# Kernel tuning notes

Measured on AMD Instinct MI355X. Metric: run time of the kernel, lower is better.

Reference implementation:

```python
import jax, jax.numpy as jnp
import numpy as np

B, T, E, D = 8, 2048, 1024, 128  # batch, seq, embedding_dim, head_dim


def setup_inputs() -> dict:
    key = jax.random.key(0)
    ks = jax.random.split(key, 7)
    s = 1.0 / np.sqrt(E)  # torch Linear default init scale
    return {
        "x": jax.random.normal(ks[0], (B, T, E), dtype=jnp.float32),
        "Wq": jax.random.uniform(ks[1], (E, D), jnp.float32, -s, s),
        "bq": jax.random.uniform(ks[2], (D,), jnp.float32, -s, s),
        "Wk": jax.random.uniform(ks[3], (E, D), jnp.float32, -s, s),
        "bk": jax.random.uniform(ks[4], (D,), jnp.float32, -s, s),
        "Wv": jax.random.uniform(ks[5], (E, D), jnp.float32, -s, s),
        "bv": jax.random.uniform(ks[6], (D,), jnp.float32, -s, s),
        "mask": 1,
    }


def reference(x, Wq, bq, Wk, bk, Wv, bv, mask):
    # Q/K/V projections: [B,T,E] @ [E,D] -> [B,T,D]
    q = x @ Wq + bq
    k = x @ Wk + bk
    v = x @ Wv + bv
    d_k = q.shape[-1]
    # scores: [B,T,T]
    scores = jnp.einsum("btd,bsd->bts", q, k) / jnp.sqrt(jnp.float32(d_k))
    if mask:  # causal masked_fill with -inf (static python flag)
        causal = jnp.tril(jnp.ones((q.shape[1], q.shape[1]), dtype=bool))
        scores = jnp.where(causal[None, :, :], scores, -jnp.inf)
    att = jax.nn.softmax(scores, axis=-1)
    # dropout p=0.0 (inference) -> identity
    return jnp.einsum("bts,bsd->btd", att, v)
```

## Files before the change

### kernel.cpp

```cpp
#include <hip/hip_runtime.h>
#include <hip/hip_bf16.h>

#define BSZ  8
#define TSEQ 2048
#define EDIM 1024
#define DDIM 128
#define MROWS (BSZ * TSEQ)
#define NQT  (TSEQ / 64)

typedef __attribute__((ext_vector_type(8))) __bf16 bf16x8;
typedef __attribute__((ext_vector_type(4))) __bf16 bf16x4;
typedef __attribute__((ext_vector_type(2))) __bf16 bf16x2;
typedef __attribute__((ext_vector_type(4))) float f32x4;

__global__ __launch_bounds__(256) void wt_kernel(
    const float* __restrict__ Wq, const float* __restrict__ Wk,
    const float* __restrict__ Wv, __bf16* __restrict__ wt)
{
    const float* W = (blockIdx.y == 0) ? Wq : (blockIdx.y == 1) ? Wk : Wv;
    __bf16* o = wt + (size_t)blockIdx.y * DDIM * EDIM;
    const int k0 = blockIdx.x * 64;
    __shared__ __align__(16) __bf16 t[64][140];
    const int tid = threadIdx.x;
    #pragma unroll
    for (int i = 0; i < 8; ++i) {
        int idx = tid + i * 256;
        int k = idx >> 5, c4 = idx & 31;
        float4 v = *(const float4*)&W[(size_t)(k0 + k) * DDIM + c4 * 4];
        bf16x4 b4;
        b4[0] = (__bf16)v.x; b4[1] = (__bf16)v.y; b4[2] = (__bf16)v.z; b4[3] = (__bf16)v.w;
        *(bf16x4*)&t[k][c4 * 4] = b4;
    }
    __syncthreads();
    #pragma unroll
    for (int i = 0; i < 4; ++i) {
        int idx = tid + i * 256;
        int n = idx >> 3, c8 = idx & 7;
        bf16x8 r;
        #pragma unroll
        for (int u = 0; u < 8; ++u) r[u] = t[c8 * 8 + u][n];
        *(bf16x8*)&o[(size_t)n * EDIM + k0 + c8 * 8] = r;
    }
}

__global__ __launch_bounds__(256) void qkv_fused_kernel(
    const float* __restrict__ x, const __bf16* __restrict__ wt,
    const float* __restrict__ bq, const float* __restrict__ bk,
    const float* __restrict__ bv,
    __bf16* __restrict__ qo, __bf16* __restrict__ ko, __bf16* __restrict__ vto)
{
    const int bid = blockIdx.x;
    const int xcd = bid & 7;
    const int h   = (bid >> 3) & 3;
    const int mt  = (bid >> 5) * 8 + xcd;
    const int m0  = mt * 64;

    __shared__ __align__(16) __bf16 a_lds[64][72];
    __shared__ __align__(16) __bf16 b_lds[96][72];

    const int tid  = threadIdx.x;
    const int lane = tid & 63;
    const int wv   = tid >> 6;
    const int wr   = wv >> 1, wc = wv & 1;
    const int cl   = lane & 15, gr = lane >> 4;

    f32x4 acc[2][3] = {};

    float4 ra[4];
    bf16x8 rb[3];
    const int arow = tid >> 4,  ac4 = tid & 15;
    const int brow = tid >> 3,  bc8 = tid & 7;

#define LOADAB(K0) do {                                                        \
    _Pragma("unroll")                                                          \
    for (int i = 0; i < 4; ++i)                                                \
        ra[i] = *(const float4*)&x[(size_t)(m0 + arow + i * 16) * EDIM + (K0) + ac4 * 4]; \
    _Pragma("unroll")                                                          \
    for (int i = 0; i < 3; ++i)                                                \
        rb[i] = *(const bf16x8*)&wt[(size_t)(h * 96 + brow + i * 32) * EDIM + (K0) + bc8 * 8]; \
  } while (0)

    LOADAB(0);

    for (int k0 = 0; k0 < EDIM; k0 += 64) {
        #pragma unroll
        for (int i = 0; i < 4; ++i) {
            bf16x4 b4;
            b4[0] = (__bf16)ra[i].x; b4[1] = (__bf16)ra[i].y;
            b4[2] = (__bf16)ra[i].z; b4[3] = (__bf16)ra[i].w;
            *(bf16x4*)&a_lds[arow + i * 16][ac4 * 4] = b4;
        }
        #pragma unroll
        for (int i = 0; i < 3; ++i)
            *(bf16x8*)&b_lds[brow + i * 32][bc8 * 8] = rb[i];
        __syncthreads();

        if (k0 + 64 < EDIM) LOADAB(k0 + 64);

        #pragma unroll
        for (int ks = 0; ks < 2; ++ks) {
            bf16x8 af[2], bfr[3];
            #pragma unroll
            for (int mi = 0; mi < 2; ++mi)
                af[mi] = *(const bf16x8*)&a_lds[wr * 32 + mi * 16 + cl][ks * 32 + gr * 8];
            #pragma unroll
            for (int ni = 0; ni < 3; ++ni)
                bfr[ni] = *(const bf16x8*)&b_lds[wc * 48 + ni * 16 + cl][ks * 32 + gr * 8];
            #pragma unroll
            for (int mi = 0; mi < 2; ++mi)
                #pragma unroll
                for (int ni = 0; ni < 3; ++ni)
                    acc[mi][ni] = __builtin_amdgcn_mfma_f32_16x16x32_bf16(
                        af[mi], bfr[ni], acc[mi][ni], 0, 0, 0);
        }
        __syncthreads();
    }
#undef LOADAB

    const float qsc = 0.08838834764831845f;
    #pragma unroll
    for (int ni = 0; ni < 3; ++ni) {
        const int nbase = h * 96 + wc * 48 + ni * 16;
        const int which = nbase >> 7;
        const int d     = (nbase & 127) + cl;
        const float* bias = (which == 0) ? bq : (which == 1) ? bk : bv;
        const float bb = bias[d];
        const float sc = (which == 0) ? qsc : 1.0f;
        #pragma unroll
        for (int mi = 0; mi < 2; ++mi) {
            const int row = m0 + wr * 32 + mi * 16 + gr * 4;
            if (which == 2) {
                bf16x4 p;
                #pragma unroll
                for (int r = 0; r < 4; ++r) p[r] = (__bf16)(acc[mi][ni][r] + bb);
                *(bf16x4*)&vto[(size_t)d * MROWS + row] = p;
            } else {
                __bf16* o = (which == 0) ? qo : ko;
                #pragma unroll
                for (int r = 0; r < 4; ++r)
                    o[(size_t)(row + r) * DDIM + d] = (__bf16)((acc[mi][ni][r] + bb) * sc);
            }
        }
    }
}

__global__ __launch_bounds__(256, 3) void attn_partial_kernel(
    const __bf16* __restrict__ Q, const __bf16* __restrict__ K,
    const __bf16* __restrict__ Vt,
    __bf16* __restrict__ partO, float* __restrict__ partM, float* __restrict__ partL,
    int PL, int NP)
{
    const int bid = blockIdx.x;
    const int b   = blockIdx.y;

    int g = 0, rem = bid;
    for (;;) {
        const int np_g = (g + 1 + PL - 1) / PL;
        if (rem < np_g) break;
        rem -= np_g; ++g;
    }
    const int qt = g, p = rem;
    const int tiles = qt + 1;
    const int np = (tiles + PL - 1) / PL;
    const int lb = tiles / np, ex = tiles % np;
    const int mylen = lb + (p < ex);
    const int start = p * lb + min(p, ex);
    const int kv_lo = start * 64;
    const int kv_hi = kv_lo + mylen * 64;

    __shared__ __align__(16) __bf16 k_lds[64][136];
    __shared__ __align__(16) __bf16 v_lds[128][72];
    __shared__ __align__(16) __bf16 p_lds[4][16][72];

    const int tid  = threadIdx.x;
    const int lane = tid & 63;
    const int w    = tid >> 6;
    const int cl   = lane & 15, gr = lane >> 4;

    const int qrow = qt * 64 + w * 16;
    const size_t bT = (size_t)b * TSEQ;

    bf16x8 qf[4];
    const __bf16* qbase = Q + (bT + qrow + cl) * DDIM;
    #pragma unroll
    for (int ks = 0; ks < 4; ++ks)
        qf[ks] = *(const bf16x8*)&qbase[ks * 32 + gr * 8];

    f32x4 acc[8] = {};
    float m1 = -__builtin_inff();
    float l1 = 0.f;

    bf16x8 rk[4], rv[4];
#define LOAD_TILE(KV0) do {                                                   \
    _Pragma("unroll")                                                         \
    for (int i = 0; i < 4; ++i) {                                             \
        int idx = tid + i * 256;                                              \
        rk[i] = *(const bf16x8*)&K[(bT + (KV0) + (idx >> 4)) * DDIM + (idx & 15) * 8]; } \
    _Pragma("unroll")                                                         \
    for (int i = 0; i < 4; ++i) {                                             \
        int idx = tid + i * 256;                                              \
        rv[i] = *(const bf16x8*)&Vt[(size_t)(idx >> 3) * MROWS + bT + (KV0) + (idx & 7) * 8]; } \
  } while (0)

    LOAD_TILE(kv_lo);

    for (int kv0 = kv_lo; kv0 < kv_hi; kv0 += 64) {
        #pragma unroll
        for (int i = 0; i < 4; ++i) {
            int idx = tid + i * 256;
            *(bf16x8*)&k_lds[idx >> 4][(idx & 15) * 8] = rk[i];
        }
        #pragma unroll
        for (int i = 0; i < 4; ++i) {
            int idx = tid + i * 256;
            *(bf16x8*)&v_lds[idx >> 3][(idx & 7) * 8] = rv[i];
        }
        __syncthreads();

        if (kv0 + 64 < kv_hi) LOAD_TILE(kv0 + 64);

        f32x4 s[4] = {};
        #pragma unroll
        for (int ks = 0; ks < 4; ++ks) {
            #pragma unroll
            for (int st = 0; st < 4; ++st) {
                bf16x8 kf = *(const bf16x8*)&k_lds[st * 16 + cl][ks * 32 + gr * 8];
                s[st] = __builtin_amdgcn_mfma_f32_16x16x32_bf16(kf, qf[ks], s[st], 0, 0, 0);
            }
        }

        if (kv0 + 63 > qrow) {
            const int kvb = kv0 + gr * 4 - qrow - cl;
            #pragma unroll
            for (int st = 0; st < 4; ++st)
                #pragma unroll
                for (int r = 0; r < 4; ++r)
                    if (kvb + st * 16 + r > 0) s[st][r] = -__builtin_inff();
        }

        float tm = fmaxf(fmaxf(fmaxf(s[0][0], s[0][1]), fmaxf(s[0][2], s[0][3])),
                         fmaxf(fmaxf(s[1][0], s[1][1]), fmaxf(s[1][2], s[1][3])));
        tm = fmaxf(tm,
             fmaxf(fmaxf(fmaxf(s[2][0], s[2][1]), fmaxf(s[2][2], s[2][3])),
                   fmaxf(fmaxf(s[3][0], s[3][1]), fmaxf(s[3][2], s[3][3]))));
        tm = fmaxf(tm, __shfl_xor(tm, 16));
        tm = fmaxf(tm, __shfl_xor(tm, 32));

        if (__any(tm > m1)) {
            const float newm = fmaxf(m1, tm);
            const float alpha = __expf(m1 - newm);
            l1 *= alpha;
            m1 = newm;
            float arec[4];
            #pragma unroll
            for (int r = 0; r < 4; ++r) arec[r] = __shfl(alpha, gr * 4 + r);
            #pragma unroll
            for (int d = 0; d < 8; ++d) {
                #pragma unroll
                for (int r = 0; r < 4; ++r) acc[d][r] *= arec[r];
            }
        }

        #pragma unroll
        for (int st = 0; st < 4; ++st) {
            #pragma unroll
            for (int u = 0; u < 2; ++u) {
                float p0 = __expf(s[st][2 * u]     - m1);
                float p1 = __expf(s[st][2 * u + 1] - m1);
                l1 += p0 + p1;
                bf16x2 pp; pp[0] = (__bf16)p0; pp[1] = (__bf16)p1;
                *(bf16x2*)&p_lds[w][cl][st * 16 + gr * 4 + 2 * u] = pp;
            }
        }

        #pragma unroll
        for (int ks2 = 0; ks2 < 2; ++ks2) {
            bf16x8 pa = *(const bf16x8*)&p_lds[w][cl][ks2 * 32 + gr * 8];
            #pragma unroll
            for (int d = 0; d < 8; ++d) {
                bf16x8 vf = *(const bf16x8*)&v_lds[d * 16 + cl][ks2 * 32 + gr * 8];
                acc[d] = __builtin_amdgcn_mfma_f32_16x16x32_bf16(pa, vf, acc[d], 0, 0, 0);
            }
        }
        __syncthreads();
    }
#undef LOAD_TILE

    const size_t pidx = (size_t)b * NP + bid;
    __bf16* po = partO + pidx * (64 * 128);
    float ls = l1;
    ls += __shfl_xor(ls, 16);
    ls += __shfl_xor(ls, 32);
    if (gr == 0) {
        partM[pidx * 64 + w * 16 + cl] = m1;
        partL[pidx * 64 + w * 16 + cl] = ls;
    }
    #pragma unroll
    for (int r = 0; r < 4; ++r) {
        const int row_l = w * 16 + gr * 4 + r;
        #pragma unroll
        for (int d = 0; d < 8; ++d)
            po[row_l * 128 + d * 16 + cl] = (__bf16)acc[d][r];
    }
}

__global__ __launch_bounds__(256) void attn_combine_kernel(
    const __bf16* __restrict__ partO, const float* __restrict__ partM,
    const float* __restrict__ partL, float* __restrict__ out, int PL, int NP)
{
    const int qt = blockIdx.x, b = blockIdx.y;
    int pre = 0;
    for (int g2 = 0; g2 < qt; ++g2) pre += (g2 + 1 + PL - 1) / PL;
    const int nv = (qt + 1 + PL - 1) / PL;
    const size_t pbase = (size_t)b * NP + pre;

    const int tid = threadIdx.x;
    const int col = (tid & 31) * 4;
    const int rbase = blockIdx.z * 32;

    #pragma unroll
    for (int rr = 0; rr < 4; ++rr) {
        const int row = rbase + (tid >> 5) + rr * 8;
        float mx = -__builtin_inff();
        for (int c = 0; c < nv; ++c)
            mx = fmaxf(mx, partM[(pbase + c) * 64 + row]);
        float lsum = 0.f;
        f32x4 o = {0.f, 0.f, 0.f, 0.f};
        for (int c = 0; c < nv; ++c) {
            const float wgt = __expf(partM[(pbase + c) * 64 + row] - mx);
            lsum += wgt * partL[(pbase + c) * 64 + row];
            const bf16x4 po = *(const bf16x4*)&partO[(pbase + c) * (64 * 128) + (size_t)row * 128 + col];
            o.x += wgt * (float)po[0]; o.y += wgt * (float)po[1];
            o.z += wgt * (float)po[2]; o.w += wgt * (float)po[3];
        }
        const float inv = 1.0f / lsum;
        f32x4 res = {o.x * inv, o.y * inv, o.z * inv, o.w * inv};
        *(f32x4*)&out[((size_t)b * TSEQ + qt * 64 + row) * DDIM + col] = res;
    }
}

extern "C" void kernel_launch(void* const* d_in, const int* in_sizes, int n_in,
                              void* d_out, int out_size, void* d_ws, size_t ws_size,
                              hipStream_t stream) {
    const float* x  = (const float*)d_in[0];
    const float* Wq = (const float*)d_in[1];
    const float* bq = (const float*)d_in[2];
    const float* Wk = (const float*)d_in[3];
    const float* bk = (const float*)d_in[4];
    const float* Wv = (const float*)d_in[5];
    const float* bv = (const float*)d_in[6];

    __bf16* q  = (__bf16*)d_ws;
    __bf16* k  = q  + (size_t)MROWS * DDIM;
    __bf16* vt = k  + (size_t)MROWS * DDIM;
    __bf16* wt = vt + (size_t)MROWS * DDIM;
    const size_t fixed_bytes = ((size_t)3 * MROWS * DDIM + (size_t)3 * DDIM * EDIM) * sizeof(__bf16);

    int PL = 4, NP = 0;
    for (int g2 = 0; g2 < NQT; ++g2) NP += (g2 + 1 + PL - 1) / PL;
    {
        const size_t need = fixed_bytes +
            (size_t)NP * BSZ * 64 * (128 * sizeof(__bf16) + 2 * sizeof(float));
        if (ws_size < need) {
            PL = 8; NP = 0;
            for (int g2 = 0; g2 < NQT; ++g2) NP += (g2 + 1 + PL - 1) / PL;
        }
    }
    __bf16* partO = (__bf16*)((char*)d_ws + fixed_bytes);
    float* partM = (float*)(partO + (size_t)NP * BSZ * 64 * 128);
    float* partL = partM + (size_t)NP * BSZ * 64;

    wt_kernel<<<dim3(EDIM / 64, 3), 256, 0, stream>>>(Wq, Wk, Wv, wt);
    qkv_fused_kernel<<<dim3((MROWS / 64) * 4), 256, 0, stream>>>(x, wt, bq, bk, bv, q, k, vt);
    attn_partial_kernel<<<dim3(NP, BSZ), 256, 0, stream>>>(q, k, vt, partO, partM, partL, PL, NP);
    attn_combine_kernel<<<dim3(NQT, BSZ, 2), 256, 0, stream>>>(partO, partM, partL,
                                                               (float*)d_out, PL, NP);
}
```

Before: 83.93 us.

## Load QKV projection tiles directly into swizzled LDS via global_load_lds

Replaces the register-staged global loads of the x and weight tiles with direct global-to-LDS loads (global_load_lds, 16 bytes per lane). The A tile is now stored as fp32 in LDS and converted to bf16 on read, and both tiles use XOR swizzling to avoid bank conflicts. The aim is to cut VGPR use and the register-to-LDS store instructions, and the launch bounds ask for 4 blocks per CU. In exchange the register prefetch of the next tile is gone, so global loads are no longer overlapped with MFMA work, and the fp32 A tile doubles its LDS footprint.

```diff
diff --git a/kernel.cpp b/kernel.cpp
--- a/kernel.cpp
+++ b/kernel.cpp
@@ -12,6 +12,11 @@
 typedef __attribute__((ext_vector_type(4))) __bf16 bf16x4;
 typedef __attribute__((ext_vector_type(2))) __bf16 bf16x2;
 typedef __attribute__((ext_vector_type(4))) float f32x4;
+
+#define GLOAD_LDS(G, L) \
+    __builtin_amdgcn_global_load_lds( \
+        (const __attribute__((address_space(1))) void*)(G), \
+        (__attribute__((address_space(3))) void*)(L), 16, 0, 0)
 
 __global__ __launch_bounds__(256) void wt_kernel(
     const float* __restrict__ Wq, const float* __restrict__ Wk,
@@ -43,7 +48,10 @@
     }
 }
 
-__global__ __launch_bounds__(256) void qkv_fused_kernel(
+#define A_LDS_BYTES 16384
+#define B_LDS_BYTES 12288
+
+__global__ __launch_bounds__(256, 4) void qkv_fused_kernel(
     const float* __restrict__ x, const __bf16* __restrict__ wt,
     const float* __restrict__ bq, const float* __restrict__ bk,
     const float* __restrict__ bv,
@@ -55,8 +63,7 @@
     const int mt  = (bid >> 5) * 8 + xcd;
     const int m0  = mt * 64;
 
-    __shared__ __align__(16) __bf16 a_lds[64][72];
-    __shared__ __align__(16) __bf16 b_lds[96][72];
+    __shared__ __align__(16) char lds[A_LDS_BYTES + B_LDS_BYTES];
 
     const int tid  = threadIdx.x;
     const int lane = tid & 63;
@@ -66,46 +73,58 @@
 
     f32x4 acc[2][3] = {};
 
-    float4 ra[4];
-    bf16x8 rb[3];
-    const int arow = tid >> 4,  ac4 = tid & 15;
-    const int brow = tid >> 3,  bc8 = tid & 7;
-
-#define LOADAB(K0) do {                                                        \
-    _Pragma("unroll")                                                          \
-    for (int i = 0; i < 4; ++i)                                                \
-        ra[i] = *(const float4*)&x[(size_t)(m0 + arow + i * 16) * EDIM + (K0) + ac4 * 4]; \
-    _Pragma("unroll")                                                          \
-    for (int i = 0; i < 3; ++i)                                                \
-        rb[i] = *(const bf16x8*)&wt[(size_t)(h * 96 + brow + i * 32) * EDIM + (K0) + bc8 * 8]; \
-  } while (0)
-
-    LOADAB(0);
+    const float* asrc[4];
+    char* adst[4];
+    #pragma unroll
+    for (int i = 0; i < 4; ++i) {
+        const int row  = i * 16 + (tid >> 4);
+        const int lcol = ((tid & 15) * 16) ^ ((row & 7) << 5);
+        asrc[i] = x + (size_t)(m0 + row) * EDIM + (lcol >> 2);
+        adst[i] = lds + i * 4096 + tid * 16;
+    }
+    const __bf16* bsrc[3];
+    char* bdst[3];
+    #pragma unroll
+    for (int i = 0; i < 3; ++i) {
+        const int row  = i * 32 + (tid >> 3);
+        const int lcol = ((tid & 7) * 16) ^ ((row & 7) << 4);
+        bsrc[i] = wt + (size_t)(h * 96 + row) * EDIM + (lcol >> 1);
+        bdst[i] = lds + A_LDS_BYTES + i * 4096 + tid * 16;
+    }
+
+    const int sa = (cl & 7) << 5;
+    const int sb = (cl & 7) << 4;
 
     for (int k0 = 0; k0 < EDIM; k0 += 64) {
         #pragma unroll
-        for (int i = 0; i < 4; ++i) {
-            bf16x4 b4;
-            b4[0] = (__bf16)ra[i].x; b4[1] = (__bf16)ra[i].y;
-            b4[2] = (__bf16)ra[i].z; b4[3] = (__bf16)ra[i].w;
-            *(bf16x4*)&a_lds[arow + i * 16][ac4 * 4] = b4;
-        }
-        #pragma unroll
-        for (int i = 0; i < 3; ++i)
-            *(bf16x8*)&b_lds[brow + i * 32][bc8 * 8] = rb[i];
+        for (int i = 0; i < 4; ++i) GLOAD_LDS(asrc[i] + k0, adst[i]);
+        #pragma unroll
+        for (int i = 0; i < 3; ++i) GLOAD_LDS(bsrc[i] + k0, bdst[i]);
         __syncthreads();
-
-        if (k0 + 64 < EDIM) LOADAB(k0 + 64);
 
         #pragma unroll
         for (int ks = 0; ks < 2; ++ks) {
             bf16x8 af[2], bfr[3];
             #pragma unroll
-            for (int mi = 0; mi < 2; ++mi)
-                af[mi] = *(const bf16x8*)&a_lds[wr * 32 + mi * 16 + cl][ks * 32 + gr * 8];
-            #pragma unroll
-            for (int ni = 0; ni < 3; ++ni)
-                bfr[ni] = *(const bf16x8*)&b_lds[wc * 48 + ni * 16 + cl][ks * 32 + gr * 8];
+            for (int mi = 0; mi < 2; ++mi) {
+                const int off = (wr * 32 + mi * 16 + cl) * 256
+                              + ((ks * 128 + gr * 32) ^ sa);
+                f32x4 lo = *(const f32x4*)(lds + off);
+                f32x4 hi = *(const f32x4*)(lds + off + 16);
+                bf16x8 t;
+                t[0] = (__bf16)lo[0]; t[1] = (__bf16)lo[1];
+                t[2] = (__bf16)lo[2]; t[3] = (__bf16)lo[3];
+                t[4] = (__bf16)hi[0]; t[5] = (__bf16)hi[1];
+                t[6] = (__bf16)hi[2]; t[7] = (__bf16)hi[3];
+                af[mi] = t;
+            }
+            #pragma unroll
+            for (int ni = 0; ni < 3; ++ni) {
+                const int off = A_LDS_BYTES
+                              + (wc * 48 + ni * 16 + cl) * 128
+                              + ((ks * 64 + gr * 16) ^ sb);
+                bfr[ni] = *(const bf16x8*)(lds + off);
+            }
             #pragma unroll
             for (int mi = 0; mi < 2; ++mi)
                 #pragma unroll
@@ -115,7 +134,6 @@
         }
         __syncthreads();
     }
-#undef LOADAB
 
     const float qsc = 0.08838834764831845f;
     #pragma unroll
```

Measured after the change: 85.03 us. About the same (+1.3%).
